# Performance work log

Hardware: AMD Instinct MI355X
Metric: run time of the kernel (lower is better)

## Reference

```python
import jax, jax.numpy as jnp
import numpy as np
from jax import lax

B, S, H = 4, 512, 2048
E, D = 16, 128
GH = E * D  # GRU hidden size = num_experts * router_dim
BAL_STRENGTH = 0.01


def _l2norm(v, eps):
    n = jnp.linalg.norm(v, axis=-1, keepdims=True)
    return v / jnp.maximum(n, eps)


def setup_inputs() -> dict:
    key = jax.random.key(0)
    ks = jax.random.split(key, 6)
    x = jax.random.normal(ks[0], (B, S, H), dtype=jnp.float32)
    hn = jax.random.normal(ks[1], (1, B, GH), dtype=jnp.float32)
    w_ih = jax.random.normal(ks[2], (3 * GH, H), dtype=jnp.float32) * 0.02
    w_hh = jax.random.normal(ks[3], (3 * GH, GH), dtype=jnp.float32) * 0.02
    w_expr = jax.random.normal(ks[4], (H, GH), dtype=jnp.float32) * 0.02
    expert_load_ema = jax.random.uniform(ks[5], (E,), dtype=jnp.float32)
    return {"x": x, "hn": hn, "w_ih": w_ih, "w_hh": w_hh,
            "w_expr": w_expr, "expert_load_ema": expert_load_ema, "top_k": 2}


def _gru(x, h0, w_ih, w_hh):
    # PyTorch GRU (no bias): gates ordered (r, z, n). Precompute input proj once.
    xi = jnp.einsum('bsh,gh->sbg', x, w_ih)  # [S,B,3*GH]
    xr, xz, xn = jnp.split(xi, 3, axis=-1)
    wr, wz, wn = jnp.split(w_hh, 3, axis=0)

    def step(h, xs):
        xr_t, xz_t, xn_t = xs
        r = jax.nn.sigmoid(xr_t + h @ wr.T)
        z = jax.nn.sigmoid(xz_t + h @ wz.T)
        n = jnp.tanh(xn_t + r * (h @ wn.T))
        h = (1.0 - z) * n + z * h
        return h, h

    hT, hs = lax.scan(step, h0, (xr, xz, xn))
    return hs.transpose(1, 0, 2), hT[None]  # [B,S,GH], [1,B,GH]


def reference(x, hn, w_ih, w_hh, w_expr, expert_load_ema, top_k):
    b, s, _ = x.shape
    e = expert_load_ema.shape[0]
    gh = w_hh.shape[1]
    d = gh // e

    routing_logits, hn_out = _gru(x, hn[0], w_ih, w_hh)

    expression_logits = (x @ w_expr).reshape(b, s, e, d)
    rout = routing_logits.reshape(b, s, e, d)
    rout = _l2norm(rout, 1e-12)  # F.normalize(dim=-1)

    # per-token expert gram matrix [B,S,E,E]
    gram = jnp.einsum('bsed,bsfd->bsef', rout, rout)
    diff = gram - jnp.eye(e, dtype=rout.dtype)
    diffn = _l2norm(diff, 1e-12)
    speciality_penalty = jnp.mean(jnp.sum(diffn ** 2, axis=(-2, -1)))

    # cosine sim (rout already unit-norm)
    en = jnp.maximum(jnp.linalg.norm(expression_logits, axis=-1), 1e-8)
    rn = jnp.maximum(jnp.linalg.norm(rout, axis=-1), 1e-8)
    cos = jnp.sum(expression_logits * rout, axis=-1) / (en * rn)
    cosine_similarities = 1.0 - cos  # [B,S,E]

    domain = (cosine_similarities * (1.0 + speciality_penalty)).reshape(b * s, e)
    top_vals, selected_experts = lax.top_k(domain, top_k)
    multiplier = jax.nn.softmax(top_vals.astype(jnp.float32), axis=-1).astype(domain.dtype)

    # ExpressionProjector orthogonal loss
    gw = w_expr.T @ w_expr
    expression_loss = jnp.mean((gw - jnp.eye(gh, dtype=w_expr.dtype)) ** 2)

    # training-mode EMA load-balance adjustment (no_grad in torch)
    ema = lax.stop_gradient(expert_load_ema)
    total = ema.sum()
    scores = jnp.where(total > 0, ema / jnp.maximum(total, 1e-12), jnp.zeros_like(ema))
    adjustment = scores * BAL_STRENGTH * e
    multiplier = multiplier - adjustment[selected_experts]

    return (multiplier, selected_experts, expression_logits, hn_out,
            speciality_penalty, cosine_similarities, expression_loss)
```

## Files before the change

kernel.cpp:

```cpp
#include <hip/hip_runtime.h>
#include <hip/hip_bf16.h>
#include <math.h>

#define BB 4
#define SS 512
#define HH 2048
#define EE 16
#define DD 128
#define GH 2048
#define G3 6144
#define NTOK 2048

#define LSTR 132
#define FPAD 32
#define KS 40

typedef __attribute__((ext_vector_type(8))) short short8;
typedef __attribute__((ext_vector_type(4))) float f32x4;

__global__ __launch_bounds__(256) void gemm_abt(const float* __restrict__ A,
                                                const float* __restrict__ B,
                                                float* __restrict__ C,
                                                int M, int N, int K) {
  __shared__ float As[8][LSTR];
  __shared__ float Bs[8][LSTR];
  const int bm = blockIdx.y * 128, bn = blockIdx.x * 128;
  const int tid = threadIdx.x;
  const int lm = tid >> 1;
  const int kh = (tid & 1) * 4;
  const int tx = tid & 15, ty = tid >> 4;
  float acc[8][8] = {};
  const float* Arow = A + (size_t)(bm + lm) * K + kh;
  const float* Brow = B + (size_t)(bn + lm) * K + kh;
  for (int k0 = 0; k0 < K; k0 += 8) {
    float4 av = *(const float4*)(Arow + k0);
    float4 bv = *(const float4*)(Brow + k0);
    As[kh + 0][lm] = av.x; As[kh + 1][lm] = av.y; As[kh + 2][lm] = av.z; As[kh + 3][lm] = av.w;
    Bs[kh + 0][lm] = bv.x; Bs[kh + 1][lm] = bv.y; Bs[kh + 2][lm] = bv.z; Bs[kh + 3][lm] = bv.w;
    __syncthreads();
#pragma unroll
    for (int kk = 0; kk < 8; ++kk) {
      float a8[8], b8[8];
      *(float4*)(a8)     = *(const float4*)(&As[kk][ty * 8]);
      *(float4*)(a8 + 4) = *(const float4*)(&As[kk][ty * 8 + 4]);
      *(float4*)(b8)     = *(const float4*)(&Bs[kk][tx * 8]);
      *(float4*)(b8 + 4) = *(const float4*)(&Bs[kk][tx * 8 + 4]);
#pragma unroll
      for (int i = 0; i < 8; ++i)
#pragma unroll
        for (int j = 0; j < 8; ++j) acc[i][j] = fmaf(a8[i], b8[j], acc[i][j]);
    }
    __syncthreads();
  }
#pragma unroll
  for (int i = 0; i < 8; ++i) {
    float4 v0 = {acc[i][0], acc[i][1], acc[i][2], acc[i][3]};
    float4 v1 = {acc[i][4], acc[i][5], acc[i][6], acc[i][7]};
    float* crow = C + (size_t)(bm + ty * 8 + i) * N + bn + tx * 8;
    *(float4*)(crow)     = v0;
    *(float4*)(crow + 4) = v1;
  }
}

__global__ __launch_bounds__(256) void gemm_ab(const float* __restrict__ A,
                                               const float* __restrict__ B,
                                               float* __restrict__ C,
                                               int M, int N, int K) {
  __shared__ float As[8][LSTR];
  __shared__ float Bs[8][LSTR];
  const int bm = blockIdx.y * 128, bn = blockIdx.x * 128;
  const int tid = threadIdx.x;
  const int lm = tid >> 1;
  const int kh = (tid & 1) * 4;
  const int bk = tid >> 5;
  const int bn4 = (tid & 31) * 4;
  const int tx = tid & 15, ty = tid >> 4;
  float acc[8][8] = {};
  const float* Arow = A + (size_t)(bm + lm) * K + kh;
  for (int k0 = 0; k0 < K; k0 += 8) {
    float4 av = *(const float4*)(Arow + k0);
    float4 bv = *(const float4*)(B + (size_t)(k0 + bk) * N + bn + bn4);
    As[kh + 0][lm] = av.x; As[kh + 1][lm] = av.y; As[kh + 2][lm] = av.z; As[kh + 3][lm] = av.w;
    *(float4*)(&Bs[bk][bn4]) = bv;
    __syncthreads();
#pragma unroll
    for (int kk = 0; kk < 8; ++kk) {
      float a8[8], b8[8];
      *(float4*)(a8)     = *(const float4*)(&As[kk][ty * 8]);
      *(float4*)(a8 + 4) = *(const float4*)(&As[kk][ty * 8 + 4]);
      *(float4*)(b8)     = *(const float4*)(&Bs[kk][tx * 8]);
      *(float4*)(b8 + 4) = *(const float4*)(&Bs[kk][tx * 8 + 4]);
#pragma unroll
      for (int i = 0; i < 8; ++i)
#pragma unroll
        for (int j = 0; j < 8; ++j) acc[i][j] = fmaf(a8[i], b8[j], acc[i][j]);
    }
    __syncthreads();
  }
#pragma unroll
  for (int i = 0; i < 8; ++i) {
    float4 v0 = {acc[i][0], acc[i][1], acc[i][2], acc[i][3]};
    float4 v1 = {acc[i][4], acc[i][5], acc[i][6], acc[i][7]};
    float* crow = C + (size_t)(bm + ty * 8 + i) * N + bn + tx * 8;
    *(float4*)(crow)     = v0;
    *(float4*)(crow + 4) = v1;
  }
}

__global__ __launch_bounds__(256) void ata_loss(const float* __restrict__ A,
                                                float* __restrict__ el_accum,
                                                int N, int K) {
  __shared__ float As[8][LSTR];
  __shared__ float Bs[8][LSTR];
  __shared__ float red[256];
  const int bi = blockIdx.y * 128, bj = blockIdx.x * 128;
  const int tid = threadIdx.x;
  const int bk = tid >> 5;
  const int bn4 = (tid & 31) * 4;
  const int tx = tid & 15, ty = tid >> 4;
  float acc[8][8] = {};
  for (int k0 = 0; k0 < K; k0 += 8) {
    float4 av = *(const float4*)(A + (size_t)(k0 + bk) * N + bi + bn4);
    float4 bv = *(const float4*)(A + (size_t)(k0 + bk) * N + bj + bn4);
    *(float4*)(&As[bk][bn4]) = av;
    *(float4*)(&Bs[bk][bn4]) = bv;
    __syncthreads();
#pragma unroll
    for (int kk = 0; kk < 8; ++kk) {
      float a8[8], b8[8];
      *(float4*)(a8)     = *(const float4*)(&As[kk][ty * 8]);
      *(float4*)(a8 + 4) = *(const float4*)(&As[kk][ty * 8 + 4]);
      *(float4*)(b8)     = *(const float4*)(&Bs[kk][tx * 8]);
      *(float4*)(b8 + 4) = *(const float4*)(&Bs[kk][tx * 8 + 4]);
#pragma unroll
      for (int i = 0; i < 8; ++i)
#pragma unroll
        for (int j = 0; j < 8; ++j) acc[i][j] = fmaf(a8[i], b8[j], acc[i][j]);
    }
    __syncthreads();
  }
  float local = 0.f;
#pragma unroll
  for (int i = 0; i < 8; ++i) {
#pragma unroll
    for (int j = 0; j < 8; ++j) {
      int gi = bi + ty * 8 + i, gj = bj + tx * 8 + j;
      float d = acc[i][j] - ((gi == gj) ? 1.0f : 0.0f);
      local += d * d;
    }
  }
  red[tid] = local;
  __syncthreads();
  for (int s = 128; s > 0; s >>= 1) {
    if (tid < s) red[tid] += red[tid + s];
    __syncthreads();
  }
  if (tid == 0) atomicAdd(el_accum, red[0]);
}

__device__ inline void bf16_split(float v, unsigned short& hi, unsigned short& lo) {
  unsigned u = __float_as_uint(v);
  unsigned r = u + 0x7FFFu + ((u >> 16) & 1u);
  hi = (unsigned short)(r >> 16);
  float rem = v - __uint_as_float((unsigned)hi << 16);
  lo = (unsigned short)(__float_as_uint(rem) >> 16);
}

__global__ __launch_bounds__(256) void split_mat(const float* __restrict__ A,
                                                 unsigned short* __restrict__ Hh,
                                                 unsigned short* __restrict__ Hl,
                                                 int n) {
  int i = blockIdx.x * 256 + threadIdx.x;
  int stride = gridDim.x * 256;
  for (; i < n; i += stride) {
    unsigned short hi, lo;
    bf16_split(A[i], hi, lo);
    Hh[i] = hi; Hl[i] = lo;
  }
}

__global__ __launch_bounds__(256) void transpose_split(const float* __restrict__ A,
                                                       unsigned short* __restrict__ Th,
                                                       unsigned short* __restrict__ Tl) {
  __shared__ float tile[64][65];
  const int bx = blockIdx.x * 64, by = blockIdx.y * 64;
  const int tx = threadIdx.x & 63, ty = threadIdx.x >> 6;
#pragma unroll
  for (int i = 0; i < 16; ++i) {
    int r = ty + i * 4;
    tile[r][tx] = A[(size_t)(by + r) * GH + bx + tx];
  }
  __syncthreads();
#pragma unroll
  for (int i = 0; i < 16; ++i) {
    int r = ty + i * 4;
    unsigned short hi, lo;
    bf16_split(tile[tx][r], hi, lo);
    Th[(size_t)(bx + r) * HH + by + tx] = hi;
    Tl[(size_t)(bx + r) * HH + by + tx] = lo;
  }
}

__global__ __launch_bounds__(256) void gemm_abt_bf16(
    const unsigned short* __restrict__ Ah, const unsigned short* __restrict__ Al,
    const unsigned short* __restrict__ Bh, const unsigned short* __restrict__ Bl,
    float* __restrict__ C, int M, int N, int K) {
  __shared__ unsigned short Ahs[128 * KS], Als[128 * KS];
  __shared__ unsigned short Bhs[128 * KS], Bls[128 * KS];
  const int tid = threadIdx.x;
  const int wv = tid >> 6, lane = tid & 63;
  const int qr = wv >> 1, qc = wv & 1;
  const int m16 = lane & 15, q = lane >> 4;
  const int bm = blockIdx.y * 128, bn = blockIdx.x * 128;
  const int sr = tid >> 1, sh = (tid & 1) * 16;
  f32x4 zero = {0.f, 0.f, 0.f, 0.f};
  f32x4 acc[4][4];
#pragma unroll
  for (int i = 0; i < 4; ++i)
#pragma unroll
    for (int j = 0; j < 4; ++j) acc[i][j] = zero;

  for (int k0 = 0; k0 < K; k0 += 32) {
    const size_t ga = (size_t)(bm + sr) * K + k0 + sh;
    const size_t gb = (size_t)(bn + sr) * K + k0 + sh;
    short8 a0 = *(const short8*)(Ah + ga);
    short8 a1 = *(const short8*)(Ah + ga + 8);
    short8 l0 = *(const short8*)(Al + ga);
    short8 l1 = *(const short8*)(Al + ga + 8);
    short8 b0 = *(const short8*)(Bh + gb);
    short8 b1 = *(const short8*)(Bh + gb + 8);
    short8 m0 = *(const short8*)(Bl + gb);
    short8 m1 = *(const short8*)(Bl + gb + 8);
    __syncthreads();
    *(short8*)&Ahs[sr * KS + sh]     = a0;
    *(short8*)&Ahs[sr * KS + sh + 8] = a1;
    *(short8*)&Als[sr * KS + sh]     = l0;
    *(short8*)&Als[sr * KS + sh + 8] = l1;
    *(short8*)&Bhs[sr * KS + sh]     = b0;
    *(short8*)&Bhs[sr * KS + sh + 8] = b1;
    *(short8*)&Bls[sr * KS + sh]     = m0;
    *(short8*)&Bls[sr * KS + sh + 8] = m1;
    __syncthreads();
    short8 afh[4], afl[4], bfh[4], bfl[4];
#pragma unroll
    for (int t = 0; t < 4; ++t) {
      const int raddr = (qr * 64 + t * 16 + m16) * KS + q * 8;
      const int caddr = (qc * 64 + t * 16 + m16) * KS + q * 8;
      afh[t] = *(const short8*)&Ahs[raddr];
      afl[t] = *(const short8*)&Als[raddr];
      bfh[t] = *(const short8*)&Bhs[caddr];
      bfl[t] = *(const short8*)&Bls[caddr];
    }
#pragma unroll
    for (int tm = 0; tm < 4; ++tm)
#pragma unroll
      for (int tn = 0; tn < 4; ++tn) {
        acc[tm][tn] = __builtin_amdgcn_mfma_f32_16x16x32_bf16(afh[tm], bfh[tn], acc[tm][tn], 0, 0, 0);
        acc[tm][tn] = __builtin_amdgcn_mfma_f32_16x16x32_bf16(afh[tm], bfl[tn], acc[tm][tn], 0, 0, 0);
        acc[tm][tn] = __builtin_amdgcn_mfma_f32_16x16x32_bf16(afl[tm], bfh[tn], acc[tm][tn], 0, 0, 0);
      }
  }
#pragma unroll
  for (int tm = 0; tm < 4; ++tm)
#pragma unroll
    for (int tn = 0; tn < 4; ++tn)
#pragma unroll
      for (int r = 0; r < 4; ++r)
        C[(size_t)(bm + qr * 64 + tm * 16 + q * 4 + r) * N +
          bn + qc * 64 + tn * 16 + m16] = acc[tm][tn][r];
}

__global__ __launch_bounds__(256) void ata_bf16(
    const unsigned short* __restrict__ Th, const unsigned short* __restrict__ Tl,
    float* __restrict__ el_accum, int N, int K) {
  __shared__ unsigned short Ahs[128 * KS], Als[128 * KS];
  __shared__ unsigned short Bhs[128 * KS], Bls[128 * KS];
  __shared__ float red[256];
  const int tid = threadIdx.x;
  const int wv = tid >> 6, lane = tid & 63;
  const int qr = wv >> 1, qc = wv & 1;
  const int m16 = lane & 15, q = lane >> 4;
  const int bi = blockIdx.y * 128, bj = blockIdx.x * 128;
  const int sr = tid >> 1, sh = (tid & 1) * 16;
  f32x4 zero = {0.f, 0.f, 0.f, 0.f};
  f32x4 acc[4][4];
#pragma unroll
  for (int i = 0; i < 4; ++i)
#pragma unroll
    for (int j = 0; j < 4; ++j) acc[i][j] = zero;

  for (int k0 = 0; k0 < K; k0 += 32) {
    const size_t ga = (size_t)(bi + sr) * K + k0 + sh;
    const size_t gb = (size_t)(bj + sr) * K + k0 + sh;
    short8 a0 = *(const short8*)(Th + ga);
    short8 a1 = *(const short8*)(Th + ga + 8);
    short8 l0 = *(const short8*)(Tl + ga);
    short8 l1 = *(const short8*)(Tl + ga + 8);
    short8 b0 = *(const short8*)(Th + gb);
    short8 b1 = *(const short8*)(Th + gb + 8);
    short8 m0 = *(const short8*)(Tl + gb);
    short8 m1 = *(const short8*)(Tl + gb + 8);
    __syncthreads();
    *(short8*)&Ahs[sr * KS + sh]     = a0;
    *(short8*)&Ahs[sr * KS + sh + 8] = a1;
    *(short8*)&Als[sr * KS + sh]     = l0;
    *(short8*)&Als[sr * KS + sh + 8] = l1;
    *(short8*)&Bhs[sr * KS + sh]     = b0;
    *(short8*)&Bhs[sr * KS + sh + 8] = b1;
    *(short8*)&Bls[sr * KS + sh]     = m0;
    *(short8*)&Bls[sr * KS + sh + 8] = m1;
    __syncthreads();
    short8 afh[4], afl[4], bfh[4], bfl[4];
#pragma unroll
    for (int t = 0; t < 4; ++t) {
      const int raddr = (qr * 64 + t * 16 + m16) * KS + q * 8;
      const int caddr = (qc * 64 + t * 16 + m16) * KS + q * 8;
      afh[t] = *(const short8*)&Ahs[raddr];
      afl[t] = *(const short8*)&Als[raddr];
      bfh[t] = *(const short8*)&Bhs[caddr];
      bfl[t] = *(const short8*)&Bls[caddr];
    }
#pragma unroll
    for (int tm = 0; tm < 4; ++tm)
#pragma unroll
      for (int tn = 0; tn < 4; ++tn) {
        acc[tm][tn] = __builtin_amdgcn_mfma_f32_16x16x32_bf16(afh[tm], bfh[tn], acc[tm][tn], 0, 0, 0);
        acc[tm][tn] = __builtin_amdgcn_mfma_f32_16x16x32_bf16(afh[tm], bfl[tn], acc[tm][tn], 0, 0, 0);
        acc[tm][tn] = __builtin_amdgcn_mfma_f32_16x16x32_bf16(afl[tm], bfh[tn], acc[tm][tn], 0, 0, 0);
      }
  }
  float local = 0.f;
#pragma unroll
  for (int tm = 0; tm < 4; ++tm)
#pragma unroll
    for (int tn = 0; tn < 4; ++tn)
#pragma unroll
      for (int r = 0; r < 4; ++r) {
        int gi = bi + qr * 64 + tm * 16 + q * 4 + r;
        int gj = bj + qc * 64 + tn * 16 + m16;
        float d = acc[tm][tn][r] - ((gi == gj) ? 1.0f : 0.0f);
        local += d * d;
      }
  red[tid] = local;
  __syncthreads();
  for (int s = 128; s > 0; s >>= 1) {
    if (tid < s) red[tid] += red[tid + s];
    __syncthreads();
  }
  if (tid == 0) atomicAdd(el_accum, red[0]);
}

__device__ inline float wred64(float v) {
#pragma unroll
  for (int o = 32; o; o >>= 1) v += __shfl_xor(v, o);
  return v;
}

__global__ __launch_bounds__(512, 2) void gru_persistent(
    const float* __restrict__ xi,
    const float* __restrict__ w_hh,
    const float* __restrict__ hn,
    float* __restrict__ hsx,
    int* __restrict__ flags) {
  __shared__ __align__(16) float hsm[BB * GH];
  const int tid = threadIdx.x;
  const int wave = tid >> 6, lane = tid & 63;
  const int j = blockIdx.x * 8 + wave;

  float wgr[32], wgz[32], wgn[32];
  {
    const float* pr = w_hh + (size_t)j * GH;
    const float* pz = w_hh + (size_t)(GH + j) * GH;
    const float* pn = w_hh + (size_t)(2 * GH + j) * GH;
#pragma unroll
    for (int c = 0; c < 32; ++c) {
      int k = c * 64 + lane;
      wgr[c] = pr[k]; wgz[c] = pz[k]; wgn[c] = pn[k];
    }
  }
#pragma unroll
  for (int i = 0; i < 4; ++i) {
    int k = tid + i * 512;
    float4 v;
    v.x = hn[0 * GH + k]; v.y = hn[1 * GH + k];
    v.z = hn[2 * GH + k]; v.w = hn[3 * GH + k];
    *(float4*)(&hsm[k * 4]) = v;
  }
  __syncthreads();

  for (int s = 0; s < SS; ++s) {
    float xr = 0.f, xz = 0.f, xn_ = 0.f;
    if (lane < BB) {
      const float* xrow = xi + ((size_t)(lane * SS + s)) * G3;
      xr  = xrow[j];
      xz  = xrow[GH + j];
      xn_ = xrow[2 * GH + j];
    }

    float ar[BB] = {}, az[BB] = {}, an[BB] = {};
#pragma unroll
    for (int c = 0; c < 32; ++c) {
      float4 h4 = *(const float4*)(&hsm[(c * 64 + lane) * 4]);
      float w_r = wgr[c], w_z = wgz[c], w_n = wgn[c];
      ar[0] = fmaf(w_r, h4.x, ar[0]); az[0] = fmaf(w_z, h4.x, az[0]); an[0] = fmaf(w_n, h4.x, an[0]);
      ar[1] = fmaf(w_r, h4.y, ar[1]); az[1] = fmaf(w_z, h4.y, az[1]); an[1] = fmaf(w_n, h4.y, an[1]);
      ar[2] = fmaf(w_r, h4.z, ar[2]); az[2] = fmaf(w_z, h4.z, az[2]); an[2] = fmaf(w_n, h4.z, an[2]);
      ar[3] = fmaf(w_r, h4.w, ar[3]); az[3] = fmaf(w_z, h4.w, az[3]); an[3] = fmaf(w_n, h4.w, an[3]);
    }
#pragma unroll
    for (int b = 0; b < BB; ++b) { ar[b] = wred64(ar[b]); az[b] = wred64(az[b]); an[b] = wred64(an[b]); }

    if (lane < BB) {
      const int b = lane;
      float r = 1.0f / (1.0f + expf(-(xr + ar[b])));
      float z = 1.0f / (1.0f + expf(-(xz + az[b])));
      float n = tanhf(xn_ + r * an[b]);
      float hp = hsm[j * 4 + b];
      float hv = (1.0f - z) * n + z * hp;
      __hip_atomic_store(hsx + (((size_t)s * 256 + blockIdx.x) * BB + b) * 8 + (j & 7),
                         hv, __ATOMIC_RELAXED, __HIP_MEMORY_SCOPE_AGENT);
    }

    if (s + 1 < SS) {
      __syncthreads();
      if (tid == 0)
        __hip_atomic_store(&flags[blockIdx.x * FPAD], s + 1,
                           __ATOMIC_RELAXED, __HIP_MEMORY_SCOPE_AGENT);
      const int p = tid >> 1;
      const int c4 = (tid & 1) * 4;
      const int want = s + 1;
      while (__hip_atomic_load(&flags[p * FPAD], __ATOMIC_RELAXED,
                               __HIP_MEMORY_SCOPE_AGENT) < want)
        __builtin_amdgcn_s_sleep(1);
      const float* line = hsx + ((size_t)s * 256 + p) * 32 + c4;
      float4 v0 = *(const float4*)(line + 0 * 8);
      float4 v1 = *(const float4*)(line + 1 * 8);
      float4 v2 = *(const float4*)(line + 2 * 8);
      float4 v3 = *(const float4*)(line + 3 * 8);
      const int k0 = tid * 4;
      *(float4*)(&hsm[(k0 + 0) * 4]) = float4{v0.x, v1.x, v2.x, v3.x};
      *(float4*)(&hsm[(k0 + 1) * 4]) = float4{v0.y, v1.y, v2.y, v3.y};
      *(float4*)(&hsm[(k0 + 2) * 4]) = float4{v0.z, v1.z, v2.z, v3.z};
      *(float4*)(&hsm[(k0 + 3) * 4]) = float4{v0.w, v1.w, v2.w, v3.w};
      __syncthreads();
    }
  }
}

__device__ inline float red16(float v) {
#pragma unroll
  for (int o = 8; o; o >>= 1) v += __shfl_xor(v, o);
  return v;
}

__global__ __launch_bounds__(256) void token_kernel(const float* __restrict__ hsx,
                                                    const float* __restrict__ expr,
                                                    float* __restrict__ cos_out,
                                                    float* __restrict__ sp_accum) {
  __shared__ float routn[EE * 132];
  __shared__ float rowc[EE];
  const int t = blockIdx.x;
  const int b = t / SS, s = t % SS;
  const int tid = threadIdx.x;
  const int e = tid >> 4, sub = tid & 15;

  const float* rrow = hsx + ((size_t)s * 256 + e * 16 + sub) * 32 + b * 8;
  float rv[8];
  *(float4*)(rv)     = *(const float4*)(rrow);
  *(float4*)(rv + 4) = *(const float4*)(rrow + 4);
  float ss = 0.f;
#pragma unroll
  for (int i = 0; i < 8; ++i) ss += rv[i] * rv[i];
  ss = red16(ss);
  float inv = 1.0f / fmaxf(sqrtf(ss), 1e-12f);
#pragma unroll
  for (int i = 0; i < 8; ++i) {
    rv[i] *= inv;
    routn[e * 132 + sub * 8 + i] = rv[i];
  }

  const float* erow = expr + (size_t)t * GH + e * DD + sub * 8;
  float en2 = 0.f, dot = 0.f;
#pragma unroll
  for (int i = 0; i < 8; ++i) {
    float ev = erow[i];
    en2 += ev * ev;
    dot += ev * rv[i];
  }
  en2 = red16(en2);
  dot = red16(dot);
  if (sub == 0) {
    float cosv = dot / fmaxf(sqrtf(en2), 1e-8f);
    cos_out[t * EE + e] = 1.0f - cosv;
  }
  __syncthreads();

  const int f = sub;
  float g = 0.f;
#pragma unroll
  for (int d = 0; d < DD; ++d)
    g = fmaf(routn[e * 132 + d], routn[f * 132 + d], g);
  float diff = g - ((e == f) ? 1.0f : 0.0f);
  float rowsum = red16(diff * diff);
  if (f == 0) {
    float nrm = fmaxf(sqrtf(rowsum), 1e-12f);
    rowc[e] = rowsum / (nrm * nrm);
  }
  __syncthreads();
  if (tid == 0) {
    float tok = 0.f;
#pragma unroll
    for (int i = 0; i < EE; ++i) tok += rowc[i];
    atomicAdd(sp_accum, tok);
  }
}

__global__ __launch_bounds__(256) void final_kernel(const float* __restrict__ hsx,
                                                    const float* __restrict__ cos_out,
                                                    const float* __restrict__ ema,
                                                    const float* __restrict__ accum,
                                                    float* __restrict__ out_mult,
                                                    float* __restrict__ out_sel,
                                                    float* __restrict__ out_hn,
                                                    float* __restrict__ out_sp,
                                                    float* __restrict__ out_el) {
  const int gtid = blockIdx.x * 256 + threadIdx.x;
  if (gtid < BB * GH) {
    int b = gtid / GH, k = gtid % GH;
    out_hn[gtid] = hsx[((size_t)(SS - 1) * 256 + (k >> 3)) * 32 + b * 8 + (k & 7)];
  }
  if (gtid < NTOK) {
    float sp = accum[0] / (float)NTOK;
    float scale = 1.0f + sp;
    float dv[EE];
#pragma unroll
    for (int e = 0; e < EE; ++e) dv[e] = cos_out[gtid * EE + e] * scale;
    int i0 = 0; float v0 = dv[0];
#pragma unroll
    for (int e = 1; e < EE; ++e) { if (dv[e] > v0) { v0 = dv[e]; i0 = e; } }
    int i1 = -1; float v1 = -1e30f;
#pragma unroll
    for (int e = 0; e < EE; ++e) { if (e != i0 && dv[e] > v1) { v1 = dv[e]; i1 = e; } }
    float ex = expf(v1 - v0);
    float den = 1.0f + ex;
    float m0 = 1.0f / den, m1 = ex / den;
    float total = 0.f;
#pragma unroll
    for (int e = 0; e < EE; ++e) total += ema[e];
    float a0 = 0.f, a1 = 0.f;
    if (total > 0.f) {
      float invt = 1.0f / fmaxf(total, 1e-12f);
      a0 = ema[i0] * invt * 0.01f * (float)EE;
      a1 = ema[i1] * invt * 0.01f * (float)EE;
    }
    out_mult[gtid * 2 + 0] = m0 - a0;
    out_mult[gtid * 2 + 1] = m1 - a1;
    out_sel[gtid * 2 + 0] = (float)i0;
    out_sel[gtid * 2 + 1] = (float)i1;
  }
  if (gtid == 0) {
    out_sp[0] = accum[0] / (float)NTOK;
    out_el[0] = accum[1] / (float)(GH * GH);
  }
}

extern "C" void kernel_launch(void* const* d_in, const int* in_sizes, int n_in,
                              void* d_out, int out_size, void* d_ws, size_t ws_size,
                              hipStream_t stream) {
  const float* x      = (const float*)d_in[0];
  const float* hn     = (const float*)d_in[1];
  const float* w_ih   = (const float*)d_in[2];
  const float* w_hh   = (const float*)d_in[3];
  const float* w_expr = (const float*)d_in[4];
  const float* ema    = (const float*)d_in[5];
  float* out = (float*)d_out;

  float* out_mult = out;
  float* out_sel  = out + 4096;
  float* out_expr = out + 8192;
  float* out_hn   = out + 4202496;
  float* out_sp   = out + 4210688;
  float* out_cos  = out + 4210689;
  float* out_el   = out + 4243457;

  float* ws = (float*)d_ws;
  float* xi    = ws;
  float* hsx   = ws + 12582912;
  float* accum = ws + 16777216;
  int*   flags = (int*)(ws + 16777220);
  unsigned short* xh  = (unsigned short*)(ws + 16785920);
  unsigned short* xl  = (unsigned short*)(ws + 18883072);
  unsigned short* wth = (unsigned short*)(ws + 20980224);
  unsigned short* wtl = (unsigned short*)(ws + 23077376);
  const size_t need_bytes = (size_t)25174528 * 4;
  const bool bf16path = ws_size >= need_bytes;

  hipMemsetAsync(accum, 0, (4 + 256 * FPAD) * sizeof(float), stream);

  gemm_abt<<<dim3(G3 / 128, NTOK / 128), 256, 0, stream>>>(x, w_ih, xi, NTOK, G3, HH);

  if (bf16path) {
    split_mat<<<4096, 256, 0, stream>>>(x, xh, xl, NTOK * HH);
    transpose_split<<<dim3(GH / 64, HH / 64), 256, 0, stream>>>(w_expr, wth, wtl);
    gemm_abt_bf16<<<dim3(GH / 128, NTOK / 128), 256, 0, stream>>>(
        xh, xl, wth, wtl, out_expr, NTOK, GH, HH);
    ata_bf16<<<dim3(GH / 128, GH / 128), 256, 0, stream>>>(wth, wtl, accum + 1, GH, HH);
  } else {
    gemm_ab<<<dim3(GH / 128, NTOK / 128), 256, 0, stream>>>(x, w_expr, out_expr, NTOK, GH, HH);
    ata_loss<<<dim3(GH / 128, GH / 128), 256, 0, stream>>>(w_expr, accum + 1, GH, HH);
  }

  {
    void* args[] = {(void*)&xi, (void*)&w_hh, (void*)&hn, (void*)&hsx, (void*)&flags};
    hipLaunchCooperativeKernel((void*)gru_persistent, dim3(256), dim3(512),
                               args, 0, stream);
  }

  token_kernel<<<NTOK, 256, 0, stream>>>(hsx, out_expr, out_cos, accum);

  final_kernel<<<(BB * GH + 255) / 256, 256, 0, stream>>>(hsx, out_cos, ema, accum,
                                                          out_mult, out_sel, out_hn,
                                                          out_sp, out_el);
}
```

Before: 3.965 ms.

## Double-buffer GRU hidden state, swizzle LDS layout, and replace barrier with arrival counter

The persistent GRU kernel now keeps two LDS copies of the hidden state, so next-step values can be written while the current copy is still being read. That lets the pre-publish __syncthreads be replaced by a shared-memory arrival counter: the last wave to finish its stores raises the block's global flag. The hidden-state LDS layout is swizzled to reduce bank conflicts on the float4 reads and writes. The first four steps of the wave reduction use DPP adds instead of shuffles. The trade-off is more LDS, which may affect the 2-block occupancy, and a more delicate memory-ordering scheme that relies on the vmcnt wait before the counter increment.

```diff
diff --git a/kernel.cpp b/kernel.cpp
--- a/kernel.cpp
+++ b/kernel.cpp
@@ -350,9 +350,18 @@
   if (tid == 0) atomicAdd(el_accum, red[0]);
 }
 
+template <int CTRL>
+__device__ inline float dpp_add(float v) {
+  int t = __builtin_amdgcn_update_dpp(0, __float_as_int(v), CTRL, 0xf, 0xf, false);
+  return v + __int_as_float(t);
+}
 __device__ inline float wred64(float v) {
-#pragma unroll
-  for (int o = 32; o; o >>= 1) v += __shfl_xor(v, o);
+  v = dpp_add<0x121>(v);
+  v = dpp_add<0x122>(v);
+  v = dpp_add<0x124>(v);
+  v = dpp_add<0x128>(v);
+  v += __shfl_xor(v, 16);
+  v += __shfl_xor(v, 32);
   return v;
 }
 
@@ -362,7 +371,8 @@
     const float* __restrict__ hn,
     float* __restrict__ hsx,
     int* __restrict__ flags) {
-  __shared__ __align__(16) float hsm[BB * GH];
+  __shared__ __align__(16) float hsm[2][BB * GH];
+  __shared__ int arrive;
   const int tid = threadIdx.x;
   const int wave = tid >> 6, lane = tid & 63;
   const int j = blockIdx.x * 8 + wave;
@@ -384,11 +394,20 @@
     float4 v;
     v.x = hn[0 * GH + k]; v.y = hn[1 * GH + k];
     v.z = hn[2 * GH + k]; v.w = hn[3 * GH + k];
-    *(float4*)(&hsm[k * 4]) = v;
-  }
+    int slot = (k & ~63) | ((k & 3) << 4) | ((k >> 2) & 15);
+    *(float4*)(&hsm[0][slot * 4]) = v;
+  }
+  if (tid == 0) arrive = 0;
   __syncthreads();
 
+  const int rdo = (((lane & 3) << 4) | (lane >> 2)) * 4;
+  const int hpo = (((j & ~63) | ((j & 3) << 4) | ((j >> 2) & 15))) * 4;
+  const int wsb = ((((tid >> 4) << 6) | (tid & 15))) * 4;
+
   for (int s = 0; s < SS; ++s) {
+    const float* cur = hsm[s & 1];
+    float* nxt = hsm[(s + 1) & 1];
+
     float xr = 0.f, xz = 0.f, xn_ = 0.f;
     if (lane < BB) {
       const float* xrow = xi + ((size_t)(lane * SS + s)) * G3;
@@ -400,7 +419,7 @@
     float ar[BB] = {}, az[BB] = {}, an[BB] = {};
 #pragma unroll
     for (int c = 0; c < 32; ++c) {
-      float4 h4 = *(const float4*)(&hsm[(c * 64 + lane) * 4]);
+      float4 h4 = *(const float4*)(cur + c * 256 + rdo);
       float w_r = wgr[c], w_z = wgz[c], w_n = wgn[c];
       ar[0] = fmaf(w_r, h4.x, ar[0]); az[0] = fmaf(w_z, h4.x, az[0]); an[0] = fmaf(w_n, h4.x, an[0]);
       ar[1] = fmaf(w_r, h4.y, ar[1]); az[1] = fmaf(w_z, h4.y, az[1]); an[1] = fmaf(w_n, h4.y, an[1]);
@@ -415,17 +434,20 @@
       float r = 1.0f / (1.0f + expf(-(xr + ar[b])));
       float z = 1.0f / (1.0f + expf(-(xz + az[b])));
       float n = tanhf(xn_ + r * an[b]);
-      float hp = hsm[j * 4 + b];
+      float hp = cur[hpo + b];
       float hv = (1.0f - z) * n + z * hp;
       __hip_atomic_store(hsx + (((size_t)s * 256 + blockIdx.x) * BB + b) * 8 + (j & 7),
                          hv, __ATOMIC_RELAXED, __HIP_MEMORY_SCOPE_AGENT);
     }
 
     if (s + 1 < SS) {
-      __syncthreads();
-      if (tid == 0)
-        __hip_atomic_store(&flags[blockIdx.x * FPAD], s + 1,
-                           __ATOMIC_RELAXED, __HIP_MEMORY_SCOPE_AGENT);
+      asm volatile("s_waitcnt vmcnt(0)" ::: "memory");
+      if (lane == 0) {
+        int old = atomicAdd(&arrive, 1);
+        if (old == 8 * (s + 1) - 1)
+          __hip_atomic_store(&flags[blockIdx.x * FPAD], s + 1,
+                             __ATOMIC_RELAXED, __HIP_MEMORY_SCOPE_AGENT);
+      }
       const int p = tid >> 1;
       const int c4 = (tid & 1) * 4;
       const int want = s + 1;
@@ -437,11 +459,10 @@
       float4 v1 = *(const float4*)(line + 1 * 8);
       float4 v2 = *(const float4*)(line + 2 * 8);
       float4 v3 = *(const float4*)(line + 3 * 8);
-      const int k0 = tid * 4;
-      *(float4*)(&hsm[(k0 + 0) * 4]) = float4{v0.x, v1.x, v2.x, v3.x};
-      *(float4*)(&hsm[(k0 + 1) * 4]) = float4{v0.y, v1.y, v2.y, v3.y};
-      *(float4*)(&hsm[(k0 + 2) * 4]) = float4{v0.z, v1.z, v2.z, v3.z};
-      *(float4*)(&hsm[(k0 + 3) * 4]) = float4{v0.w, v1.w, v2.w, v3.w};
+      *(float4*)(nxt + wsb +   0) = float4{v0.x, v1.x, v2.x, v3.x};
+      *(float4*)(nxt + wsb +  64) = float4{v0.y, v1.y, v2.y, v3.y};
+      *(float4*)(nxt + wsb + 128) = float4{v0.z, v1.z, v2.z, v3.z};
+      *(float4*)(nxt + wsb + 192) = float4{v0.w, v1.w, v2.w, v3.w};
       __syncthreads();
     }
   }
```

Result: slower. 4.864 ms (+22.7%).
